# Kernel optimization log

Measured on AMD Instinct MI355X. Metric: run time of the kernel, lower is better.

Reference implementation:

```python
import jax, jax.numpy as jnp
import numpy as np

B, S, D, H = 4, 1024, 1024, 16
DK = D // H


def _linear_params(key, scale):
    kw, kb = jax.random.split(key)
    W = jax.random.normal(kw, (D, D), dtype=jnp.float32) * scale
    b = jax.random.normal(kb, (D,), dtype=jnp.float32) * 0.01
    return W, b


def setup_inputs() -> dict:
    key = jax.random.key(0)
    ks = jax.random.split(key, 12)
    scale = 1.0 / np.sqrt(D)
    inp = {
        "query": jax.random.normal(ks[0], (B, S, D), dtype=jnp.float32),
        "key": jax.random.normal(ks[1], (B, S, D), dtype=jnp.float32),
        "value": jax.random.normal(ks[2], (B, S, D), dtype=jnp.float32),
        "time_k": jax.random.normal(ks[3], (B, S, D), dtype=jnp.float32),
        "time_v": jax.random.normal(ks[4], (B, S, D), dtype=jnp.float32),
        "mask": jnp.zeros((B, 1, S, S), dtype=jnp.float32),
    }
    names = ["Wq", "bq", "Wk", "bk", "Wv", "bv", "Wtk", "btk", "Wtv", "btv", "Wm", "bm"]
    for i in range(6):
        W, b = _linear_params(ks[5 + i], scale)
        inp[names[2 * i]] = W
        inp[names[2 * i + 1]] = b
    return inp


def _split_heads(x):
    # [B,S,D] -> [B,H,S,DK]
    b, s, _ = x.shape
    return x.reshape(b, s, H, DK).transpose(0, 2, 1, 3)


def reference(query, key, value, time_k, time_v, mask,
              Wq, bq, Wk, bk, Wv, bv, Wtk, btk, Wtv, btv, Wm, bm):
    q = _split_heads(query @ Wq + bq)
    k = _split_heads(key @ Wk + bk)
    v = _split_heads(value @ Wv + bv)
    t_k = _split_heads(time_k @ Wtk + btk)
    t_v = _split_heads(time_v @ Wtv + btv)

    # scores[b,h,i,j] = q_i . k_j + t_k_i . q_j  (note second term uses q on the key axis)
    scores = jnp.einsum("bhid,bhjd->bhij", q, k) + jnp.einsum("bhid,bhjd->bhij", t_k, q)
    # module divides by sqrt(d_model) (query.size(-1)), not sqrt(d_k)
    scores = scores / jnp.sqrt(jnp.float32(D)) + mask
    probs = jax.nn.softmax(scores, axis=-1)

    # dropout is identity (p=0 / eval); squeeze(-2) is a no-op for S>1
    context = jnp.einsum("bhij,bhjd->bhid", probs, v) + jnp.einsum("bhij,bhjd->bhid", probs, t_v)
    x = context.transpose(0, 2, 1, 3).reshape(query.shape[0], -1, D)
    return x @ Wm + bm
```

## Files before the change

### kernel.cpp

```cpp
#include <hip/hip_runtime.h>
#include <hip/hip_bf16.h>
#include <cstdint>
#include <cstddef>

typedef __bf16 bf16;
typedef bf16 bf16x8 __attribute__((ext_vector_type(8)));
typedef bf16 bf16x4 __attribute__((ext_vector_type(4)));
typedef float f32x4 __attribute__((ext_vector_type(4)));
typedef unsigned int u32;

#define DEV static __device__ __forceinline__

DEV f32x4 mfma16(bf16x8 a, bf16x8 b, f32x4 c) {
    return __builtin_amdgcn_mfma_f32_16x16x32_bf16(a, b, c, 0, 0, 0);
}

DEV f32x4 shflx4(f32x4 v, int m) {
    f32x4 r;
    for (int i = 0; i < 4; ++i) r[i] = __shfl_xor(v[i], m, 64);
    return r;
}

DEV bf16x8 cvt8(const float* p) {
    float4 f0 = *(const float4*)p;
    float4 f1 = *(const float4*)(p + 4);
    bf16x8 v;
    v[0] = (bf16)f0.x; v[1] = (bf16)f0.y; v[2] = (bf16)f0.z; v[3] = (bf16)f0.w;
    v[4] = (bf16)f1.x; v[5] = (bf16)f1.y; v[6] = (bf16)f1.z; v[7] = (bf16)f1.w;
    return v;
}

DEV void glo(const bf16* g, bf16* l) {
    __builtin_amdgcn_global_load_lds(
        (const __attribute__((address_space(1))) u32*)g,
        (__attribute__((address_space(3))) u32*)l,
        16, 0, 0);
}

struct PrepArgs {
    const float* w[6];
    const float* act[5];
    bf16* wt;
    bf16* actbf[5];
};

__global__ __launch_bounds__(256) void prep_kernel(PrepArgs p)
{
    const int z = blockIdx.z;
    const int t = threadIdx.x;
    if (z < 6) {
        __shared__ bf16 tile[64][72];
        const float* src = p.w[z];
        bf16* out = p.wt + (size_t)z * 1024 * 1024;
        const int r = t >> 3, c8 = (t & 7) * 8;
        const int row0 = blockIdx.y * 64, col0 = blockIdx.x * 64;
        *(bf16x8*)&tile[r][c8]      = cvt8(&src[(size_t)(row0 + r) * 1024 + col0 + c8]);
        *(bf16x8*)&tile[r + 32][c8] = cvt8(&src[(size_t)(row0 + r + 32) * 1024 + col0 + c8]);
        __syncthreads();
        for (int half = 0; half < 2; ++half) {
            int rr = r + half * 32;
            bf16x8 v;
            for (int j = 0; j < 8; ++j) v[j] = tile[c8 + j][rr];
            *(bf16x8*)&out[(size_t)(col0 + rr) * 1024 + row0 + c8] = v;
        }
    } else {
        const float* src = p.act[z - 6];
        bf16* dst = p.actbf[z - 6];
        const size_t chunk = (size_t)(blockIdx.y * 16 + blockIdx.x) * 16384;
        for (int c = 0; c < 8; ++c) {
            const size_t off = chunk + (size_t)c * 2048 + (size_t)t * 8;
            *(bf16x8*)&dst[off] = cvt8(&src[off]);
        }
    }
}

struct ProjArgs {
    const void* A[5];
    const void* A2[5];
    const bf16* W[5];
    const bf16* W2[5];
    const float* bias[5];
    const float* bias2[5];
    bf16* out[5];
    int vst[5];
};

template<bool AF32>
__global__ __launch_bounds__(256) void proj_gemm(ProjArgs pa)
{
    const int z = blockIdx.z;
    const void* A   = pa.A[z];
    const void* A2p = pa.A2[z];
    const bf16* W   = pa.W[z];
    const bf16* W2  = pa.W2[z];
    const int m0 = blockIdx.y * 128, n0 = blockIdx.x * 128;
    __shared__ bf16 As[128 * 64];
    __shared__ bf16 Bs[128 * 64];
    const int t = threadIdx.x, lane = t & 63, w = t >> 6;
    const int ln = lane & 15, qd = lane >> 4;
    const int wm0 = (w >> 1) * 64, wn0 = (w & 1) * 64;
    const int srow = t >> 1, shalf = (t & 1) * 32;
    const int sub0 = w * 4;
    const int r8 = lane >> 3, c8 = (lane & 7) * 8;
    f32x4 acc[4][4];
    for (int i = 0; i < 4; ++i)
        for (int j = 0; j < 4; ++j)
            acc[i][j] = (f32x4){0.f, 0.f, 0.f, 0.f};
    const int npair = A2p ? 2 : 1;
    for (int pair = 0; pair < npair; ++pair) {
        const void* Ap = pair ? A2p : A;
        const bf16* Wp = pair ? W2 : W;
        for (int ks = 0; ks < 16; ++ks) {
            const int bk = ks * 64;
            __syncthreads();
            for (int i = 0; i < 4; ++i) {
                const int row = (sub0 + i) * 8 + r8;
                glo(&Wp[(size_t)(n0 + row) * 1024 + bk + c8], &Bs[(sub0 + i) * 512]);
            }
            if (AF32) {
                const float* src = &((const float*)Ap)[(size_t)(m0 + srow) * 1024 + bk + shalf];
                bf16* dst = &As[srow * 64 + shalf];
                *(bf16x8*)(dst)      = cvt8(src);
                *(bf16x8*)(dst + 8)  = cvt8(src + 8);
                *(bf16x8*)(dst + 16) = cvt8(src + 16);
                *(bf16x8*)(dst + 24) = cvt8(src + 24);
            } else {
                const bf16* Ab = (const bf16*)Ap;
                for (int i = 0; i < 4; ++i) {
                    const int row = (sub0 + i) * 8 + r8;
                    glo(&Ab[(size_t)(m0 + row) * 1024 + bk + c8], &As[(sub0 + i) * 512]);
                }
            }
            __syncthreads();
            for (int kc = 0; kc < 2; ++kc) {
                bf16x8 af[4], bfr[4];
                for (int mi = 0; mi < 4; ++mi)
                    af[mi] = *(const bf16x8*)&As[(wm0 + mi * 16 + ln) * 64 + kc * 32 + qd * 8];
                for (int ni = 0; ni < 4; ++ni)
                    bfr[ni] = *(const bf16x8*)&Bs[(wn0 + ni * 16 + ln) * 64 + kc * 32 + qd * 8];
                for (int mi = 0; mi < 4; ++mi)
                    for (int ni = 0; ni < 4; ++ni)
                        acc[mi][ni] = mfma16(af[mi], bfr[ni], acc[mi][ni]);
            }
        }
    }
    const float* bias  = pa.bias[z];
    const float* bias2 = pa.bias2[z];
    bf16* out = pa.out[z];
    const int vst = pa.vst[z];
    for (int ni = 0; ni < 4; ++ni) {
        const int n = n0 + wn0 + ni * 16 + ln;
        const float bv = bias[n] + (bias2 ? bias2[n] : 0.0f);
        for (int mi = 0; mi < 4; ++mi) {
            const int mbase = m0 + wm0 + mi * 16 + qd * 4;
            f32x4 v = acc[mi][ni];
            if (vst) {
                const int b = mbase >> 10, s = mbase & 1023;
                bf16x4 pk;
                for (int r = 0; r < 4; ++r) pk[r] = (bf16)(v[r] + bv);
                *(bf16x4*)&out[((size_t)(b * 1024 + n)) * 1024 + s] = pk;
            } else {
                for (int r = 0; r < 4; ++r)
                    out[(size_t)(mbase + r) * 1024 + n] = (bf16)(v[r] + bv);
            }
        }
    }
}

template<bool VADD>
__global__ __launch_bounds__(256, 4) void attn3_kernel(
    const bf16* __restrict__ Qb, const bf16* __restrict__ Kb, const bf16* __restrict__ TKb,
    const bf16* __restrict__ Va, const bf16* __restrict__ Vb,
    const float* __restrict__ mask, bf16* __restrict__ ctx)
{
    const int h = blockIdx.x, it = blockIdx.y, b = blockIdx.z;
    const int i0 = it * 64;
    __shared__ bf16 Ks[64 * 64];
    __shared__ bf16 QJs[64 * 64];
    __shared__ bf16 Vs[64 * 64];
    __shared__ bf16 Ps[64][72];
    const int t = threadIdx.x, lane = t & 63, w = t >> 6;
    const int ln = lane & 15, qd = lane >> 4;
    const size_t baseQ = ((size_t)b * 1024) * 1024 + (size_t)h * 64;

    bf16x8 qf[2], tkf[2];
    {
        const size_t row = (size_t)(i0 + w * 16 + ln);
        for (int kc = 0; kc < 2; ++kc) {
            qf[kc]  = *(const bf16x8*)&Qb [baseQ + row * 1024 + kc * 32 + qd * 8];
            tkf[kc] = *(const bf16x8*)&TKb[baseQ + row * 1024 + kc * 32 + qd * 8];
        }
    }

    f32x4 O[4];
    f32x4 psum = (f32x4){0.f, 0.f, 0.f, 0.f};
    for (int dc = 0; dc < 4; ++dc) O[dc] = (f32x4){0.f, 0.f, 0.f, 0.f};

    const float c1 = 0.045084439f;
    const float c2 = 1.442695041f;

    for (int jt = 0; jt < 16; ++jt) {
        const int j0 = jt * 64;
        __syncthreads();
        const int rr = lane >> 3, cb = (lane & 7) * 8;
        if (VADD) {
            for (int i = 0; i < 4; ++i) {
                const int u = w * 4 + i, tile = u >> 3, sub = u & 7;
                const int r8 = sub * 8 + rr;
                if (tile == 0)
                    glo(&Kb[baseQ + (size_t)(j0 + r8) * 1024 + cb], &Ks[sub * 512]);
                else
                    glo(&Qb[baseQ + (size_t)(j0 + r8) * 1024 + cb], &QJs[sub * 512]);
            }
            const int vr = t >> 2, vc = (t & 3) * 16;
            const size_t vrow = ((size_t)b * 1024 + h * 64 + vr) * 1024 + j0;
            for (int cp = 0; cp < 2; ++cp) {
                const int col = vc + cp * 8;
                bf16x8 a = *(const bf16x8*)&Va[vrow + col];
                bf16x8 bb = *(const bf16x8*)&Vb[vrow + col];
                bf16x8 s;
                for (int e = 0; e < 8; ++e) s[e] = (bf16)((float)a[e] + (float)bb[e]);
                *(bf16x8*)&Vs[vr * 64 + col] = s;
            }
        } else {
            for (int i = 0; i < 6; ++i) {
                const int u = w * 6 + i, tile = u >> 3, sub = u & 7;
                const int r8 = sub * 8 + rr;
                if (tile == 0)
                    glo(&Kb[baseQ + (size_t)(j0 + r8) * 1024 + cb], &Ks[sub * 512]);
                else if (tile == 1)
                    glo(&Qb[baseQ + (size_t)(j0 + r8) * 1024 + cb], &QJs[sub * 512]);
                else
                    glo(&Va[((size_t)b * 1024 + h * 64 + r8) * 1024 + j0 + cb], &Vs[sub * 512]);
            }
        }
        float mreg[4][4];
        const int ib = i0 + w * 16 + qd * 4;
        for (int jc = 0; jc < 4; ++jc)
            for (int r = 0; r < 4; ++r)
                mreg[jc][r] = mask[((size_t)b * 1024 + (ib + r)) * 1024 + j0 + jc * 16 + ln];
        __syncthreads();

        f32x4 sc[4];
        for (int jc = 0; jc < 4; ++jc) {
            bf16x8 kf[2], qjf[2];
            for (int kc = 0; kc < 2; ++kc) {
                kf[kc]  = *(const bf16x8*)&Ks [(jc * 16 + ln) * 64 + kc * 32 + qd * 8];
                qjf[kc] = *(const bf16x8*)&QJs[(jc * 16 + ln) * 64 + kc * 32 + qd * 8];
            }
            f32x4 a = (f32x4){0.f, 0.f, 0.f, 0.f};
            a = mfma16(qf[0], kf[0], a);
            a = mfma16(qf[1], kf[1], a);
            a = mfma16(tkf[0], qjf[0], a);
            a = mfma16(tkf[1], qjf[1], a);
            sc[jc] = a;
        }
        const int ibl = w * 16 + qd * 4;
        for (int jc = 0; jc < 4; ++jc) {
            const int jl = jc * 16 + ln;
            for (int r = 0; r < 4; ++r) {
                float p = exp2f(fmaf(sc[jc][r], c1, mreg[jc][r] * c2));
                psum[r] += p;
                Ps[ibl + r][jl] = (bf16)p;
            }
        }
        for (int kc = 0; kc < 2; ++kc) {
            bf16x8 pa = *(const bf16x8*)&Ps[w * 16 + ln][kc * 32 + qd * 8];
            for (int dc = 0; dc < 4; ++dc) {
                bf16x8 vf = *(const bf16x8*)&Vs[(dc * 16 + ln) * 64 + kc * 32 + qd * 8];
                O[dc] = mfma16(pa, vf, O[dc]);
            }
        }
    }

    for (int m = 1; m <= 8; m <<= 1) psum += shflx4(psum, m);
    f32x4 rl;
    for (int r = 0; r < 4; ++r) rl[r] = 1.0f / psum[r];
    const int ibase = i0 + w * 16 + qd * 4;
    for (int dc = 0; dc < 4; ++dc) {
        const int d = h * 64 + dc * 16 + ln;
        f32x4 v = O[dc] * rl;
        for (int r = 0; r < 4; ++r)
            ctx[((size_t)b * 1024 + ibase + r) * 1024 + d] = (bf16)v[r];
    }
}

__global__ __launch_bounds__(256) void out_gemm(
    const bf16* __restrict__ A, const bf16* __restrict__ W,
    const float* __restrict__ bias, float* __restrict__ out)
{
    const int n0 = blockIdx.x * 128, m0 = blockIdx.y * 64;
    __shared__ bf16 As[64 * 64];
    __shared__ bf16 Bs[128 * 64];
    const int t = threadIdx.x, lane = t & 63, w = t >> 6;
    const int ln = lane & 15, qd = lane >> 4;
    const int wn0 = w * 32;
    const int rr = lane >> 3, cb = (lane & 7) * 8;
    f32x4 acc[4][2];
    for (int i = 0; i < 4; ++i)
        for (int j = 0; j < 2; ++j)
            acc[i][j] = (f32x4){0.f, 0.f, 0.f, 0.f};
    for (int ks = 0; ks < 16; ++ks) {
        const int bk = ks * 64;
        __syncthreads();
        for (int i = 0; i < 6; ++i) {
            const int u = w * 6 + i;
            if (u < 8) {
                const int r8 = u * 8 + rr;
                glo(&A[(size_t)(m0 + r8) * 1024 + bk + cb], &As[u * 512]);
            } else {
                const int sub = u - 8, r8 = sub * 8 + rr;
                glo(&W[(size_t)(n0 + r8) * 1024 + bk + cb], &Bs[sub * 512]);
            }
        }
        __syncthreads();
        for (int kc = 0; kc < 2; ++kc) {
            bf16x8 af[4], bfr[2];
            for (int mi = 0; mi < 4; ++mi)
                af[mi] = *(const bf16x8*)&As[(mi * 16 + ln) * 64 + kc * 32 + qd * 8];
            for (int ni = 0; ni < 2; ++ni)
                bfr[ni] = *(const bf16x8*)&Bs[(wn0 + ni * 16 + ln) * 64 + kc * 32 + qd * 8];
            for (int mi = 0; mi < 4; ++mi)
                for (int ni = 0; ni < 2; ++ni)
                    acc[mi][ni] = mfma16(af[mi], bfr[ni], acc[mi][ni]);
        }
    }
    for (int ni = 0; ni < 2; ++ni) {
        const int n = n0 + wn0 + ni * 16 + ln;
        const float bv = bias[n];
        for (int mi = 0; mi < 4; ++mi) {
            const int mbase = m0 + mi * 16 + qd * 4;
            f32x4 v = acc[mi][ni];
            for (int r = 0; r < 4; ++r)
                out[(size_t)(mbase + r) * 1024 + n] = v[r] + bv;
        }
    }
}

extern "C" void kernel_launch(void* const* d_in, const int* in_sizes, int n_in,
                              void* d_out, int out_size, void* d_ws, size_t ws_size,
                              hipStream_t stream)
{
    (void)in_sizes; (void)n_in; (void)out_size;
    const float* query  = (const float*)d_in[0];
    const float* key    = (const float*)d_in[1];
    const float* value  = (const float*)d_in[2];
    const float* time_k = (const float*)d_in[3];
    const float* time_v = (const float*)d_in[4];
    const float* mask   = (const float*)d_in[5];
    const float* Wq  = (const float*)d_in[6];  const float* bq  = (const float*)d_in[7];
    const float* Wk  = (const float*)d_in[8];  const float* bk  = (const float*)d_in[9];
    const float* Wv  = (const float*)d_in[10]; const float* bv  = (const float*)d_in[11];
    const float* Wtk = (const float*)d_in[12]; const float* btk = (const float*)d_in[13];
    const float* Wtv = (const float*)d_in[14]; const float* btv = (const float*)d_in[15];
    const float* Wm  = (const float*)d_in[16]; const float* bm  = (const float*)d_in[17];

    bf16* ws = (bf16*)d_ws;
    const size_t MM = (size_t)1024 * 1024;
    bf16* WT = ws;

    PrepArgs pp;
    pp.w[0] = Wq; pp.w[1] = Wk; pp.w[2] = Wv; pp.w[3] = Wtk; pp.w[4] = Wtv; pp.w[5] = Wm;
    pp.wt = WT;
    pp.act[0] = query; pp.act[1] = key; pp.act[2] = value;
    pp.act[3] = time_k; pp.act[4] = time_v;

    const bool big = ws_size >= (size_t)(46 * MM * sizeof(bf16));

    if (big) {
        bf16* qbf  = ws + 6 * MM;
        bf16* kbf  = ws + 10 * MM;
        bf16* vbf  = ws + 14 * MM;
        bf16* tkbf = ws + 18 * MM;
        bf16* tvbf = ws + 22 * MM;
        bf16* Qb   = ws + 26 * MM;
        bf16* Kb   = ws + 30 * MM;
        bf16* TKb  = ws + 34 * MM;
        bf16* VsTa = ws + 38 * MM;
        bf16* VsTb = ws + 42 * MM;
        bf16* ctx  = ws + 6 * MM;
        pp.actbf[0] = qbf; pp.actbf[1] = kbf; pp.actbf[2] = vbf;
        pp.actbf[3] = tkbf; pp.actbf[4] = tvbf;
        prep_kernel<<<dim3(16, 16, 11), 256, 0, stream>>>(pp);

        ProjArgs pa;
        for (int i = 0; i < 5; ++i) { pa.A2[i] = nullptr; pa.W2[i] = nullptr; pa.bias2[i] = nullptr; }
        pa.A[0] = qbf;  pa.W[0] = WT + 0 * MM; pa.bias[0] = bq;  pa.out[0] = Qb;   pa.vst[0] = 0;
        pa.A[1] = kbf;  pa.W[1] = WT + 1 * MM; pa.bias[1] = bk;  pa.out[1] = Kb;   pa.vst[1] = 0;
        pa.A[2] = tkbf; pa.W[2] = WT + 3 * MM; pa.bias[2] = btk; pa.out[2] = TKb;  pa.vst[2] = 0;
        pa.A[3] = vbf;  pa.W[3] = WT + 2 * MM; pa.bias[3] = bv;  pa.out[3] = VsTa; pa.vst[3] = 1;
        pa.A[4] = tvbf; pa.W[4] = WT + 4 * MM; pa.bias[4] = btv; pa.out[4] = VsTb; pa.vst[4] = 1;
        proj_gemm<false><<<dim3(8, 32, 5), 256, 0, stream>>>(pa);

        attn3_kernel<true><<<dim3(16, 16, 4), 256, 0, stream>>>(
            Qb, Kb, TKb, VsTa, VsTb, mask, ctx);
        out_gemm<<<dim3(8, 64), 256, 0, stream>>>(ctx, WT + 5 * MM, bm, (float*)d_out);
    } else {
        bf16* Qb  = ws + 6 * MM;
        bf16* Kb  = ws + 10 * MM;
        bf16* TKb = ws + 14 * MM;
        bf16* VsT = ws + 18 * MM;
        bf16* ctx = ws + 22 * MM;
        pp.actbf[0] = nullptr; pp.actbf[1] = nullptr; pp.actbf[2] = nullptr;
        pp.actbf[3] = nullptr; pp.actbf[4] = nullptr;
        prep_kernel<<<dim3(16, 16, 6), 256, 0, stream>>>(pp);

        ProjArgs pa;
        for (int i = 0; i < 5; ++i) { pa.A2[i] = nullptr; pa.W2[i] = nullptr; pa.bias2[i] = nullptr; }
        pa.A[0] = value;  pa.A2[0] = time_v; pa.W[0] = WT + 2 * MM; pa.W2[0] = WT + 4 * MM;
        pa.bias[0] = bv;  pa.bias2[0] = btv; pa.out[0] = VsT; pa.vst[0] = 1;
        pa.A[1] = query;  pa.W[1] = WT + 0 * MM; pa.bias[1] = bq;  pa.out[1] = Qb;  pa.vst[1] = 0;
        pa.A[2] = key;    pa.W[2] = WT + 1 * MM; pa.bias[2] = bk;  pa.out[2] = Kb;  pa.vst[2] = 0;
        pa.A[3] = time_k; pa.W[3] = WT + 3 * MM; pa.bias[3] = btk; pa.out[3] = TKb; pa.vst[3] = 0;
        proj_gemm<true><<<dim3(8, 32, 4), 256, 0, stream>>>(pa);

        attn3_kernel<false><<<dim3(16, 16, 4), 256, 0, stream>>>(
            Qb, Kb, TKb, VsT, nullptr, mask, ctx);
        out_gemm<<<dim3(8, 64), 256, 0, stream>>>(ctx, WT + 5 * MM, bm, (float*)d_out);
    }
}
```

Baseline: 335.2 us.

## Double attention row tile, stage bf16 mask in LDS, presum V outside attention

The attention kernel now processes 128 query rows per block (two 16-row subtiles per wave), so each K/Q/V tile loaded into LDS is reused twice. The mask is converted to bf16 in the prep kernel, stored temporarily in the output buffer, and loaded into LDS with global_load_lds instead of strided fp32 loads. The V+time_v sum moves from inside the attention loop into a separate elementwise kernel. The cost is more LDS and registers per block, the removed occupancy hint, an extra launch, and a bf16 approximation of the mask.

```diff
diff --git a/kernel.cpp b/kernel.cpp
--- a/kernel.cpp
+++ b/kernel.cpp
@@ -39,9 +39,9 @@
 
 struct PrepArgs {
     const float* w[6];
-    const float* act[5];
+    const float* act[6];
     bf16* wt;
-    bf16* actbf[5];
+    bf16* actbf[6];
 };
 
 __global__ __launch_bounds__(256) void prep_kernel(PrepArgs p)
@@ -71,6 +71,19 @@
             const size_t off = chunk + (size_t)c * 2048 + (size_t)t * 8;
             *(bf16x8*)&dst[off] = cvt8(&src[off]);
         }
+    }
+}
+
+__global__ __launch_bounds__(256) void vsum_kernel(bf16* __restrict__ a,
+                                                   const bf16* __restrict__ b)
+{
+    const size_t off = ((size_t)blockIdx.x * 256 + threadIdx.x) * 16;
+    for (int c = 0; c < 2; ++c) {
+        bf16x8 x = *(const bf16x8*)&a[off + c * 8];
+        bf16x8 y = *(const bf16x8*)&b[off + c * 8];
+        bf16x8 s;
+        for (int e = 0; e < 8; ++e) s[e] = (bf16)((float)x[e] + (float)y[e]);
+        *(bf16x8*)&a[off + c * 8] = s;
     }
 }
 
@@ -167,34 +180,38 @@
     }
 }
 
-template<bool VADD>
-__global__ __launch_bounds__(256, 4) void attn3_kernel(
+__global__ __launch_bounds__(256) void attn4_kernel(
     const bf16* __restrict__ Qb, const bf16* __restrict__ Kb, const bf16* __restrict__ TKb,
-    const bf16* __restrict__ Va, const bf16* __restrict__ Vb,
-    const float* __restrict__ mask, bf16* __restrict__ ctx)
+    const bf16* __restrict__ VsT, const bf16* __restrict__ maskbf,
+    bf16* __restrict__ ctx)
 {
     const int h = blockIdx.x, it = blockIdx.y, b = blockIdx.z;
-    const int i0 = it * 64;
+    const int i0 = it * 128;
     __shared__ bf16 Ks[64 * 64];
     __shared__ bf16 QJs[64 * 64];
     __shared__ bf16 Vs[64 * 64];
-    __shared__ bf16 Ps[64][72];
+    __shared__ bf16 Ms[128 * 64];
+    __shared__ bf16 Ps[128][72];
     const int t = threadIdx.x, lane = t & 63, w = t >> 6;
     const int ln = lane & 15, qd = lane >> 4;
     const size_t baseQ = ((size_t)b * 1024) * 1024 + (size_t)h * 64;
-
-    bf16x8 qf[2], tkf[2];
-    {
-        const size_t row = (size_t)(i0 + w * 16 + ln);
+    const size_t MMc = (size_t)1024 * 1024;
+
+    bf16x8 qf[2][2], tkf[2][2];
+    for (int si = 0; si < 2; ++si) {
+        const size_t row = (size_t)(i0 + w * 32 + si * 16 + ln);
         for (int kc = 0; kc < 2; ++kc) {
-            qf[kc]  = *(const bf16x8*)&Qb [baseQ + row * 1024 + kc * 32 + qd * 8];
-            tkf[kc] = *(const bf16x8*)&TKb[baseQ + row * 1024 + kc * 32 + qd * 8];
-        }
-    }
-
-    f32x4 O[4];
-    f32x4 psum = (f32x4){0.f, 0.f, 0.f, 0.f};
-    for (int dc = 0; dc < 4; ++dc) O[dc] = (f32x4){0.f, 0.f, 0.f, 0.f};
+            qf[si][kc]  = *(const bf16x8*)&Qb [baseQ + row * 1024 + kc * 32 + qd * 8];
+            tkf[si][kc] = *(const bf16x8*)&TKb[baseQ + row * 1024 + kc * 32 + qd * 8];
+        }
+    }
+
+    f32x4 O[2][4];
+    f32x4 psum[2];
+    for (int si = 0; si < 2; ++si) {
+        psum[si] = (f32x4){0.f, 0.f, 0.f, 0.f};
+        for (int dc = 0; dc < 4; ++dc) O[si][dc] = (f32x4){0.f, 0.f, 0.f, 0.f};
+    }
 
     const float c1 = 0.045084439f;
     const float c2 = 1.442695041f;
@@ -202,86 +219,79 @@
     for (int jt = 0; jt < 16; ++jt) {
         const int j0 = jt * 64;
         __syncthreads();
-        const int rr = lane >> 3, cb = (lane & 7) * 8;
-        if (VADD) {
-            for (int i = 0; i < 4; ++i) {
-                const int u = w * 4 + i, tile = u >> 3, sub = u & 7;
-                const int r8 = sub * 8 + rr;
-                if (tile == 0)
-                    glo(&Kb[baseQ + (size_t)(j0 + r8) * 1024 + cb], &Ks[sub * 512]);
-                else
-                    glo(&Qb[baseQ + (size_t)(j0 + r8) * 1024 + cb], &QJs[sub * 512]);
-            }
-            const int vr = t >> 2, vc = (t & 3) * 16;
-            const size_t vrow = ((size_t)b * 1024 + h * 64 + vr) * 1024 + j0;
-            for (int cp = 0; cp < 2; ++cp) {
-                const int col = vc + cp * 8;
-                bf16x8 a = *(const bf16x8*)&Va[vrow + col];
-                bf16x8 bb = *(const bf16x8*)&Vb[vrow + col];
-                bf16x8 s;
-                for (int e = 0; e < 8; ++e) s[e] = (bf16)((float)a[e] + (float)bb[e]);
-                *(bf16x8*)&Vs[vr * 64 + col] = s;
-            }
-        } else {
-            for (int i = 0; i < 6; ++i) {
-                const int u = w * 6 + i, tile = u >> 3, sub = u & 7;
-                const int r8 = sub * 8 + rr;
-                if (tile == 0)
-                    glo(&Kb[baseQ + (size_t)(j0 + r8) * 1024 + cb], &Ks[sub * 512]);
-                else if (tile == 1)
-                    glo(&Qb[baseQ + (size_t)(j0 + r8) * 1024 + cb], &QJs[sub * 512]);
-                else
-                    glo(&Va[((size_t)b * 1024 + h * 64 + r8) * 1024 + j0 + cb], &Vs[sub * 512]);
-            }
-        }
-        float mreg[4][4];
-        const int ib = i0 + w * 16 + qd * 4;
-        for (int jc = 0; jc < 4; ++jc)
-            for (int r = 0; r < 4; ++r)
-                mreg[jc][r] = mask[((size_t)b * 1024 + (ib + r)) * 1024 + j0 + jc * 16 + ln];
+        {
+            const int rr = lane >> 3, cb = (lane & 7) * 8;
+            for (int i = 0; i < 10; ++i) {
+                const int u = w * 10 + i;
+                if (u < 8) {
+                    glo(&Kb[baseQ + (size_t)(j0 + u * 8 + rr) * 1024 + cb], &Ks[u * 512]);
+                } else if (u < 16) {
+                    const int s = u - 8;
+                    glo(&Qb[baseQ + (size_t)(j0 + s * 8 + rr) * 1024 + cb], &QJs[s * 512]);
+                } else if (u < 24) {
+                    const int s = u - 16;
+                    glo(&VsT[((size_t)b * 1024 + h * 64 + s * 8 + rr) * 1024 + j0 + cb],
+                        &Vs[s * 512]);
+                } else {
+                    const int s = u - 24;
+                    glo(&maskbf[(size_t)b * MMc + (size_t)(i0 + s * 8 + rr) * 1024 + j0 + cb],
+                        &Ms[s * 512]);
+                }
+            }
+        }
         __syncthreads();
 
-        f32x4 sc[4];
+        f32x4 sc[2][4];
         for (int jc = 0; jc < 4; ++jc) {
             bf16x8 kf[2], qjf[2];
             for (int kc = 0; kc < 2; ++kc) {
                 kf[kc]  = *(const bf16x8*)&Ks [(jc * 16 + ln) * 64 + kc * 32 + qd * 8];
                 qjf[kc] = *(const bf16x8*)&QJs[(jc * 16 + ln) * 64 + kc * 32 + qd * 8];
             }
-            f32x4 a = (f32x4){0.f, 0.f, 0.f, 0.f};
-            a = mfma16(qf[0], kf[0], a);
-            a = mfma16(qf[1], kf[1], a);
-            a = mfma16(tkf[0], qjf[0], a);
-            a = mfma16(tkf[1], qjf[1], a);
-            sc[jc] = a;
-        }
-        const int ibl = w * 16 + qd * 4;
-        for (int jc = 0; jc < 4; ++jc) {
-            const int jl = jc * 16 + ln;
-            for (int r = 0; r < 4; ++r) {
-                float p = exp2f(fmaf(sc[jc][r], c1, mreg[jc][r] * c2));
-                psum[r] += p;
-                Ps[ibl + r][jl] = (bf16)p;
+            for (int si = 0; si < 2; ++si) {
+                f32x4 a = (f32x4){0.f, 0.f, 0.f, 0.f};
+                a = mfma16(qf[si][0], kf[0], a);
+                a = mfma16(qf[si][1], kf[1], a);
+                a = mfma16(tkf[si][0], qjf[0], a);
+                a = mfma16(tkf[si][1], qjf[1], a);
+                sc[si][jc] = a;
+            }
+        }
+        for (int si = 0; si < 2; ++si) {
+            const int ibl = w * 32 + si * 16 + qd * 4;
+            for (int jc = 0; jc < 4; ++jc) {
+                const int jl = jc * 16 + ln;
+                for (int r = 0; r < 4; ++r) {
+                    const float mv = (float)Ms[(ibl + r) * 64 + jl];
+                    const float p = exp2f(fmaf(sc[si][jc][r], c1, mv * c2));
+                    psum[si][r] += p;
+                    Ps[ibl + r][jl] = (bf16)p;
+                }
             }
         }
         for (int kc = 0; kc < 2; ++kc) {
-            bf16x8 pa = *(const bf16x8*)&Ps[w * 16 + ln][kc * 32 + qd * 8];
-            for (int dc = 0; dc < 4; ++dc) {
-                bf16x8 vf = *(const bf16x8*)&Vs[(dc * 16 + ln) * 64 + kc * 32 + qd * 8];
-                O[dc] = mfma16(pa, vf, O[dc]);
-            }
-        }
-    }
-
-    for (int m = 1; m <= 8; m <<= 1) psum += shflx4(psum, m);
-    f32x4 rl;
-    for (int r = 0; r < 4; ++r) rl[r] = 1.0f / psum[r];
-    const int ibase = i0 + w * 16 + qd * 4;
-    for (int dc = 0; dc < 4; ++dc) {
-        const int d = h * 64 + dc * 16 + ln;
-        f32x4 v = O[dc] * rl;
-        for (int r = 0; r < 4; ++r)
-            ctx[((size_t)b * 1024 + ibase + r) * 1024 + d] = (bf16)v[r];
+            bf16x8 pa[2], vb[4];
+            for (int si = 0; si < 2; ++si)
+                pa[si] = *(const bf16x8*)&Ps[w * 32 + si * 16 + ln][kc * 32 + qd * 8];
+            for (int dc = 0; dc < 4; ++dc)
+                vb[dc] = *(const bf16x8*)&Vs[(dc * 16 + ln) * 64 + kc * 32 + qd * 8];
+            for (int si = 0; si < 2; ++si)
+                for (int dc = 0; dc < 4; ++dc)
+                    O[si][dc] = mfma16(pa[si], vb[dc], O[si][dc]);
+        }
+    }
+
+    for (int si = 0; si < 2; ++si) {
+        for (int m = 1; m <= 8; m <<= 1) psum[si] += shflx4(psum[si], m);
+        f32x4 rl;
+        for (int r = 0; r < 4; ++r) rl[r] = 1.0f / psum[si][r];
+        const int ibase = i0 + w * 32 + si * 16 + qd * 4;
+        for (int dc = 0; dc < 4; ++dc) {
+            const int d = h * 64 + dc * 16 + ln;
+            f32x4 v = O[si][dc] * rl;
+            for (int r = 0; r < 4; ++r)
+                ctx[((size_t)b * 1024 + ibase + r) * 1024 + d] = (bf16)v[r];
+        }
     }
 }
 
@@ -358,12 +368,11 @@
     bf16* ws = (bf16*)d_ws;
     const size_t MM = (size_t)1024 * 1024;
     bf16* WT = ws;
+    bf16* maskbf = (bf16*)d_out;
 
     PrepArgs pp;
     pp.w[0] = Wq; pp.w[1] = Wk; pp.w[2] = Wv; pp.w[3] = Wtk; pp.w[4] = Wtv; pp.w[5] = Wm;
     pp.wt = WT;
-    pp.act[0] = query; pp.act[1] = key; pp.act[2] = value;
-    pp.act[3] = time_k; pp.act[4] = time_v;
 
     const bool big = ws_size >= (size_t)(46 * MM * sizeof(bf16));
 
@@ -379,9 +388,11 @@
         bf16* VsTa = ws + 38 * MM;
         bf16* VsTb = ws + 42 * MM;
         bf16* ctx  = ws + 6 * MM;
+        pp.act[0] = query; pp.act[1] = key; pp.act[2] = value;
+        pp.act[3] = time_k; pp.act[4] = time_v; pp.act[5] = mask;
         pp.actbf[0] = qbf; pp.actbf[1] = kbf; pp.actbf[2] = vbf;
-        pp.actbf[3] = tkbf; pp.actbf[4] = tvbf;
-        prep_kernel<<<dim3(16, 16, 11), 256, 0, stream>>>(pp);
+        pp.actbf[3] = tkbf; pp.actbf[4] = tvbf; pp.actbf[5] = maskbf;
+        prep_kernel<<<dim3(16, 16, 12), 256, 0, stream>>>(pp);
 
         ProjArgs pa;
         for (int i = 0; i < 5; ++i) { pa.A2[i] = nullptr; pa.W2[i] = nullptr; pa.bias2[i] = nullptr; }
@@ -392,8 +403,9 @@
         pa.A[4] = tvbf; pa.W[4] = WT + 4 * MM; pa.bias[4] = btv; pa.out[4] = VsTb; pa.vst[4] = 1;
         proj_gemm<false><<<dim3(8, 32, 5), 256, 0, stream>>>(pa);
 
-        attn3_kernel<true><<<dim3(16, 16, 4), 256, 0, stream>>>(
-            Qb, Kb, TKb, VsTa, VsTb, mask, ctx);
+        vsum_kernel<<<dim3(1024), 256, 0, stream>>>(VsTa, VsTb);
+        attn4_kernel<<<dim3(16, 8, 4), 256, 0, stream>>>(
+            Qb, Kb, TKb, VsTa, maskbf, ctx);
         out_gemm<<<dim3(8, 64), 256, 0, stream>>>(ctx, WT + 5 * MM, bm, (float*)d_out);
     } else {
         bf16* Qb  = ws + 6 * MM;
@@ -401,9 +413,11 @@
         bf16* TKb = ws + 14 * MM;
         bf16* VsT = ws + 18 * MM;
         bf16* ctx = ws + 22 * MM;
-        pp.actbf[0] = nullptr; pp.actbf[1] = nullptr; pp.actbf[2] = nullptr;
-        pp.actbf[3] = nullptr; pp.actbf[4] = nullptr;
-        prep_kernel<<<dim3(16, 16, 6), 256, 0, stream>>>(pp);
+        pp.act[0] = mask;
+        for (int i = 1; i < 6; ++i) pp.act[i] = nullptr;
+        pp.actbf[0] = maskbf;
+        for (int i = 1; i < 6; ++i) pp.actbf[i] = nullptr;
+        prep_kernel<<<dim3(16, 16, 7), 256, 0, stream>>>(pp);
 
         ProjArgs pa;
         for (int i = 0; i < 5; ++i) { pa.A2[i] = nullptr; pa.W2[i] = nullptr; pa.bias2[i] = nullptr; }
@@ -414,8 +428,8 @@
         pa.A[3] = time_k; pa.W[3] = WT + 3 * MM; pa.bias[3] = btk; pa.out[3] = TKb; pa.vst[3] = 0;
         proj_gemm<true><<<dim3(8, 32, 4), 256, 0, stream>>>(pa);
 
-        attn3_kernel<false><<<dim3(16, 16, 4), 256, 0, stream>>>(
-            Qb, Kb, TKb, VsT, nullptr, mask, ctx);
+        attn4_kernel<<<dim3(16, 8, 4), 256, 0, stream>>>(
+            Qb, Kb, TKb, VsT, maskbf, ctx);
         out_gemm<<<dim3(8, 64), 256, 0, stream>>>(ctx, WT + 5 * MM, bm, (float*)d_out);
     }
 }
```

After: 344.3 us. 2.7% more time.

## Precompute transposed bf16 mask and summed V before attention kernel

Applied to the files above, without the earlier changes.

The mask is converted to bf16 and transposed in the prep kernel, with the result staged in the output buffer, so the attention kernel loads it as a contiguous bf16x4 vector instead of sixteen strided fp32 loads. V and time_v projections are summed once by a separate vsum kernel, so attention loads one V tile through global_load_lds instead of adding two tiles per block. The Ps padding also changes to 68, with split bf16x4 reads. This adds an extra kernel launch and the mask transpose pass, and rounds the mask to bf16.

```diff
diff --git a/kernel.cpp b/kernel.cpp
--- a/kernel.cpp
+++ b/kernel.cpp
@@ -38,9 +38,10 @@
 }
 
 struct PrepArgs {
-    const float* w[6];
+    const float* w[10];
     const float* act[5];
     bf16* wt;
+    bf16* maskt;
     bf16* actbf[5];
 };
 
@@ -48,10 +49,11 @@
 {
     const int z = blockIdx.z;
     const int t = threadIdx.x;
-    if (z < 6) {
+    if (z < 10) {
         __shared__ bf16 tile[64][72];
         const float* src = p.w[z];
-        bf16* out = p.wt + (size_t)z * 1024 * 1024;
+        bf16* out = (z < 6) ? (p.wt + (size_t)z * 1024 * 1024)
+                            : (p.maskt + (size_t)(z - 6) * 1024 * 1024);
         const int r = t >> 3, c8 = (t & 7) * 8;
         const int row0 = blockIdx.y * 64, col0 = blockIdx.x * 64;
         *(bf16x8*)&tile[r][c8]      = cvt8(&src[(size_t)(row0 + r) * 1024 + col0 + c8]);
@@ -64,13 +66,26 @@
             *(bf16x8*)&out[(size_t)(col0 + rr) * 1024 + row0 + c8] = v;
         }
     } else {
-        const float* src = p.act[z - 6];
-        bf16* dst = p.actbf[z - 6];
+        const float* src = p.act[z - 10];
+        bf16* dst = p.actbf[z - 10];
         const size_t chunk = (size_t)(blockIdx.y * 16 + blockIdx.x) * 16384;
         for (int c = 0; c < 8; ++c) {
             const size_t off = chunk + (size_t)c * 2048 + (size_t)t * 8;
             *(bf16x8*)&dst[off] = cvt8(&src[off]);
         }
+    }
+}
+
+__global__ __launch_bounds__(256) void vsum_kernel(bf16* __restrict__ a,
+                                                   const bf16* __restrict__ b)
+{
+    const size_t off = ((size_t)blockIdx.x * 256 + threadIdx.x) * 16;
+    for (int c = 0; c < 2; ++c) {
+        bf16x8 x = *(const bf16x8*)&a[off + c * 8];
+        bf16x8 y = *(const bf16x8*)&b[off + c * 8];
+        bf16x8 s;
+        for (int e = 0; e < 8; ++e) s[e] = (bf16)((float)x[e] + (float)y[e]);
+        *(bf16x8*)&a[off + c * 8] = s;
     }
 }
 
@@ -167,21 +182,21 @@
     }
 }
 
-template<bool VADD>
-__global__ __launch_bounds__(256, 4) void attn3_kernel(
+__global__ __launch_bounds__(256, 4) void attn5_kernel(
     const bf16* __restrict__ Qb, const bf16* __restrict__ Kb, const bf16* __restrict__ TKb,
-    const bf16* __restrict__ Va, const bf16* __restrict__ Vb,
-    const float* __restrict__ mask, bf16* __restrict__ ctx)
+    const bf16* __restrict__ VsT, const bf16* __restrict__ maskT,
+    bf16* __restrict__ ctx)
 {
     const int h = blockIdx.x, it = blockIdx.y, b = blockIdx.z;
     const int i0 = it * 64;
     __shared__ bf16 Ks[64 * 64];
     __shared__ bf16 QJs[64 * 64];
     __shared__ bf16 Vs[64 * 64];
-    __shared__ bf16 Ps[64][72];
+    __shared__ bf16 Ps[64][68];
     const int t = threadIdx.x, lane = t & 63, w = t >> 6;
     const int ln = lane & 15, qd = lane >> 4;
     const size_t baseQ = ((size_t)b * 1024) * 1024 + (size_t)h * 64;
+    const size_t MMc = (size_t)1024 * 1024;
 
     bf16x8 qf[2], tkf[2];
     {
@@ -202,43 +217,29 @@
     for (int jt = 0; jt < 16; ++jt) {
         const int j0 = jt * 64;
         __syncthreads();
-        const int rr = lane >> 3, cb = (lane & 7) * 8;
-        if (VADD) {
-            for (int i = 0; i < 4; ++i) {
-                const int u = w * 4 + i, tile = u >> 3, sub = u & 7;
-                const int r8 = sub * 8 + rr;
-                if (tile == 0)
-                    glo(&Kb[baseQ + (size_t)(j0 + r8) * 1024 + cb], &Ks[sub * 512]);
-                else
-                    glo(&Qb[baseQ + (size_t)(j0 + r8) * 1024 + cb], &QJs[sub * 512]);
-            }
-            const int vr = t >> 2, vc = (t & 3) * 16;
-            const size_t vrow = ((size_t)b * 1024 + h * 64 + vr) * 1024 + j0;
-            for (int cp = 0; cp < 2; ++cp) {
-                const int col = vc + cp * 8;
-                bf16x8 a = *(const bf16x8*)&Va[vrow + col];
-                bf16x8 bb = *(const bf16x8*)&Vb[vrow + col];
-                bf16x8 s;
-                for (int e = 0; e < 8; ++e) s[e] = (bf16)((float)a[e] + (float)bb[e]);
-                *(bf16x8*)&Vs[vr * 64 + col] = s;
-            }
-        } else {
+        {
+            const int rr = lane >> 3, cb = (lane & 7) * 8;
             for (int i = 0; i < 6; ++i) {
-                const int u = w * 6 + i, tile = u >> 3, sub = u & 7;
-                const int r8 = sub * 8 + rr;
-                if (tile == 0)
-                    glo(&Kb[baseQ + (size_t)(j0 + r8) * 1024 + cb], &Ks[sub * 512]);
-                else if (tile == 1)
-                    glo(&Qb[baseQ + (size_t)(j0 + r8) * 1024 + cb], &QJs[sub * 512]);
-                else
-                    glo(&Va[((size_t)b * 1024 + h * 64 + r8) * 1024 + j0 + cb], &Vs[sub * 512]);
-            }
-        }
-        float mreg[4][4];
-        const int ib = i0 + w * 16 + qd * 4;
-        for (int jc = 0; jc < 4; ++jc)
-            for (int r = 0; r < 4; ++r)
-                mreg[jc][r] = mask[((size_t)b * 1024 + (ib + r)) * 1024 + j0 + jc * 16 + ln];
+                const int u = w * 6 + i;
+                if (u < 8) {
+                    glo(&Kb[baseQ + (size_t)(j0 + u * 8 + rr) * 1024 + cb], &Ks[u * 512]);
+                } else if (u < 16) {
+                    const int s = u - 8;
+                    glo(&Qb[baseQ + (size_t)(j0 + s * 8 + rr) * 1024 + cb], &QJs[s * 512]);
+                } else {
+                    const int s = u - 16;
+                    glo(&VsT[((size_t)b * 1024 + h * 64 + s * 8 + rr) * 1024 + j0 + cb],
+                        &Vs[s * 512]);
+                }
+            }
+        }
+        bf16x4 mv[4];
+        {
+            const int ibase = i0 + w * 16 + qd * 4;
+            for (int jc = 0; jc < 4; ++jc)
+                mv[jc] = *(const bf16x4*)&maskT[(size_t)b * MMc +
+                          (size_t)(j0 + jc * 16 + ln) * 1024 + ibase];
+        }
         __syncthreads();
 
         f32x4 sc[4];
@@ -259,13 +260,16 @@
         for (int jc = 0; jc < 4; ++jc) {
             const int jl = jc * 16 + ln;
             for (int r = 0; r < 4; ++r) {
-                float p = exp2f(fmaf(sc[jc][r], c1, mreg[jc][r] * c2));
+                const float p = exp2f(fmaf(sc[jc][r], c1, (float)mv[jc][r] * c2));
                 psum[r] += p;
                 Ps[ibl + r][jl] = (bf16)p;
             }
         }
         for (int kc = 0; kc < 2; ++kc) {
-            bf16x8 pa = *(const bf16x8*)&Ps[w * 16 + ln][kc * 32 + qd * 8];
+            bf16x4 lo = *(const bf16x4*)&Ps[w * 16 + ln][kc * 32 + qd * 8];
+            bf16x4 hi = *(const bf16x4*)&Ps[w * 16 + ln][kc * 32 + qd * 8 + 4];
+            bf16x8 pa;
+            for (int e = 0; e < 4; ++e) { pa[e] = lo[e]; pa[4 + e] = hi[e]; }
             for (int dc = 0; dc < 4; ++dc) {
                 bf16x8 vf = *(const bf16x8*)&Vs[(dc * 16 + ln) * 64 + kc * 32 + qd * 8];
                 O[dc] = mfma16(pa, vf, O[dc]);
@@ -358,12 +362,13 @@
     bf16* ws = (bf16*)d_ws;
     const size_t MM = (size_t)1024 * 1024;
     bf16* WT = ws;
+    bf16* maskT = (bf16*)d_out;
 
     PrepArgs pp;
     pp.w[0] = Wq; pp.w[1] = Wk; pp.w[2] = Wv; pp.w[3] = Wtk; pp.w[4] = Wtv; pp.w[5] = Wm;
+    for (int b = 0; b < 4; ++b) pp.w[6 + b] = mask + (size_t)b * MM;
     pp.wt = WT;
-    pp.act[0] = query; pp.act[1] = key; pp.act[2] = value;
-    pp.act[3] = time_k; pp.act[4] = time_v;
+    pp.maskt = maskT;
 
     const bool big = ws_size >= (size_t)(46 * MM * sizeof(bf16));
 
@@ -379,9 +384,11 @@
         bf16* VsTa = ws + 38 * MM;
         bf16* VsTb = ws + 42 * MM;
         bf16* ctx  = ws + 6 * MM;
+        pp.act[0] = query; pp.act[1] = key; pp.act[2] = value;
+        pp.act[3] = time_k; pp.act[4] = time_v;
         pp.actbf[0] = qbf; pp.actbf[1] = kbf; pp.actbf[2] = vbf;
         pp.actbf[3] = tkbf; pp.actbf[4] = tvbf;
-        prep_kernel<<<dim3(16, 16, 11), 256, 0, stream>>>(pp);
+        prep_kernel<<<dim3(16, 16, 15), 256, 0, stream>>>(pp);
 
         ProjArgs pa;
         for (int i = 0; i < 5; ++i) { pa.A2[i] = nullptr; pa.W2[i] = nullptr; pa.bias2[i] = nullptr; }
@@ -392,8 +399,9 @@
         pa.A[4] = tvbf; pa.W[4] = WT + 4 * MM; pa.bias[4] = btv; pa.out[4] = VsTb; pa.vst[4] = 1;
         proj_gemm<false><<<dim3(8, 32, 5), 256, 0, stream>>>(pa);
 
-        attn3_kernel<true><<<dim3(16, 16, 4), 256, 0, stream>>>(
-            Qb, Kb, TKb, VsTa, VsTb, mask, ctx);
+        vsum_kernel<<<dim3(1024), 256, 0, stream>>>(VsTa, VsTb);
+        attn5_kernel<<<dim3(16, 16, 4), 256, 0, stream>>>(
+            Qb, Kb, TKb, VsTa, maskT, ctx);
         out_gemm<<<dim3(8, 64), 256, 0, stream>>>(ctx, WT + 5 * MM, bm, (float*)d_out);
     } else {
         bf16* Qb  = ws + 6 * MM;
@@ -401,9 +409,8 @@
         bf16* TKb = ws + 14 * MM;
         bf16* VsT = ws + 18 * MM;
         bf16* ctx = ws + 22 * MM;
-        pp.actbf[0] = nullptr; pp.actbf[1] = nullptr; pp.actbf[2] = nullptr;
-        pp.actbf[3] = nullptr; pp.actbf[4] = nullptr;
-        prep_kernel<<<dim3(16, 16, 6), 256, 0, stream>>>(pp);
+        for (int i = 0; i < 5; ++i) { pp.act[i] = nullptr; pp.actbf[i] = nullptr; }
+        prep_kernel<<<dim3(16, 16, 10), 256, 0, stream>>>(pp);
 
         ProjArgs pa;
         for (int i = 0; i < 5; ++i) { pa.A2[i] = nullptr; pa.W2[i] = nullptr; pa.bias2[i] = nullptr; }
@@ -414,8 +421,8 @@
         pa.A[3] = time_k; pa.W[3] = WT + 3 * MM; pa.bias[3] = btk; pa.out[3] = TKb; pa.vst[3] = 0;
         proj_gemm<true><<<dim3(8, 32, 4), 256, 0, stream>>>(pa);
 
-        attn3_kernel<false><<<dim3(16, 16, 4), 256, 0, stream>>>(
-            Qb, Kb, TKb, VsT, nullptr, mask, ctx);
+        attn5_kernel<<<dim3(16, 16, 4), 256, 0, stream>>>(
+            Qb, Kb, TKb, VsT, maskT, ctx);
         out_gemm<<<dim3(8, 64), 256, 0, stream>>>(ctx, WT + 5 * MM, bm, (float*)d_out);
     }
 }
```

Result: slower. 342.9 us (+2.3%).
